# Performance work log

Measured on AMD Instinct MI355X. Metric: run time of the kernel, lower is better.

## Reference

```python
import jax, jax.numpy as jnp
import numpy as np

N = 262144  # points per batch (~4096 rays x 64 samples)
FDIM = 64   # plane feature dim
S = 512     # base plane resolution


def setup_inputs() -> dict:
    key = jax.random.key(0)
    ks = jax.random.split(key, 10)
    x = jax.random.uniform(ks[0], (N, 3), dtype=jnp.float32, minval=-1.0, maxval=1.0)
    rays_o = jnp.array([[0.0, 0.0, 1.5]], dtype=jnp.float32)  # ray origin; distances straddle 1.5/2.0
    scale = jnp.ones((3,), dtype=jnp.float32)
    plane = lambda k, s: jax.random.normal(k, (FDIM, s, s), dtype=jnp.float32)
    return {
        'x': x, 'rays_o': rays_o, 'scale': scale,
        'xy_plane': plane(ks[1], S), 'yz_plane': plane(ks[2], S), 'xz_plane': plane(ks[3], S),
        'xy_plane1': plane(ks[4], S // 2), 'yz_plane1': plane(ks[5], S // 2), 'xz_plane1': plane(ks[6], S // 2),
        'xy_plane2': plane(ks[7], S // 4), 'yz_plane2': plane(ks[8], S // 4), 'xz_plane2': plane(ks[9], S // 4),
    }


def bilinear_sample(plane, coords):
    """F.grid_sample(mode='bilinear', align_corners=True, padding_mode='zeros').
    plane: [C, H, W]; coords: [N, 2] with (x, y) in [-1, 1] (x indexes W).
    Returns [N, C]."""
    C, H, W = plane.shape
    fx = (coords[:, 0] + 1.0) * 0.5 * (W - 1)
    fy = (coords[:, 1] + 1.0) * 0.5 * (H - 1)
    x0 = jnp.floor(fx)
    y0 = jnp.floor(fy)
    wx = fx - x0
    wy = fy - y0
    x0i = x0.astype(jnp.int32)
    y0i = y0.astype(jnp.int32)

    def gather(xi, yi):
        valid = (xi >= 0) & (xi < W) & (yi >= 0) & (yi < H)
        xc = jnp.clip(xi, 0, W - 1)
        yc = jnp.clip(yi, 0, H - 1)
        v = plane[:, yc, xc]  # [C, N]
        return jnp.where(valid[None, :], v, 0.0)

    v00 = gather(x0i, y0i)
    v01 = gather(x0i + 1, y0i)
    v10 = gather(x0i, y0i + 1)
    v11 = gather(x0i + 1, y0i + 1)
    out = (v00 * (1 - wx) * (1 - wy) + v01 * wx * (1 - wy)
           + v10 * (1 - wx) * wy + v11 * wx * wy)  # [C, N]
    return out.T


def forward(x, rays_o, scale, xy0, yz0, xz0, xy1, yz1, xz1, xy2, yz2, xz2):
    xs = x * scale[None, :]
    xy_c = xs[:, :2]                                   # (x, y)
    xz_c = jnp.stack([xs[:, 0], xs[:, 2]], axis=-1)    # (x, z)
    yz_c = xs[:, 1:]                                   # (y, z)

    # laplace breakpoints: first index with distance > 1.5 / > 2.0 from rays_o[0]
    d = jnp.linalg.norm(rays_o[0][None, :] - xs, axis=-1)
    c1 = d > 1.5
    c2 = d > 2.0
    break1 = jnp.where(c1.any(), jnp.argmax(c1), 0)
    break2 = jnp.where(c2.any(), jnp.argmax(c2), 0)
    idx = jnp.arange(x.shape[0])
    # level 0: [0, break1), level 1: [break1, break2), level 2: [break2, N)
    level = jnp.where(idx < break1, 0, jnp.where(idx < break2, 1, 2))[:, None]

    def tri(p0, p1, p2, c):
        s0 = bilinear_sample(p0, c)
        s1 = bilinear_sample(p1, c)
        s2 = bilinear_sample(p2, c)
        # laplace: level1 = fine + half, level2 = fine + half + quarter
        return jnp.where(level == 0, s0, jnp.where(level == 1, s0 + s1, s0 + s1 + s2))

    return (tri(xy0, xy1, xy2, xy_c)
            + tri(xz0, xz1, xz2, xz_c)
            + tri(yz0, yz1, yz2, yz_c))


def reference(x, rays_o, scale, xy_plane, yz_plane, xz_plane, xy_plane1, yz_plane1, xz_plane1, xy_plane2, yz_plane2, xz_plane2):
    return forward(x, rays_o, scale, xy_plane, yz_plane, xz_plane,
                   xy_plane1, yz_plane1, xz_plane1,
                   xy_plane2, yz_plane2, xz_plane2)
```

## Files before the change

### kernel.cpp

```cpp
#include <hip/hip_runtime.h>
#include <hip/hip_fp16.h>

#define NPTS 262144
#define FDIM 64
#define NCELL 32768

typedef float vfloat4 __attribute__((ext_vector_type(4)));

__global__ __launch_bounds__(256) void break_kernel(const float* __restrict__ x,
                                                    const float* __restrict__ rays_o,
                                                    const float* __restrict__ scale,
                                                    unsigned* __restrict__ breaks) {
  const unsigned t = blockIdx.x * 256u + threadIdx.x;
  const float r0 = rays_o[0], r1 = rays_o[1], r2 = rays_o[2];
  const float s0 = scale[0], s1 = scale[1], s2 = scale[2];
  unsigned b1 = 0xFFFFFFFFu, b2 = 0xFFFFFFFFu;
  for (unsigned p = t; p < NPTS; p += 65536u) {
    const float dx = r0 - x[p * 3 + 0] * s0;
    const float dy = r1 - x[p * 3 + 1] * s1;
    const float dz = r2 - x[p * 3 + 2] * s2;
    const float d = sqrtf(__fadd_rn(__fadd_rn(__fmul_rn(dx, dx), __fmul_rn(dy, dy)),
                                    __fmul_rn(dz, dz)));
    if (d > 1.5f) b1 = min(b1, p);
    if (d > 2.0f) b2 = min(b2, p);
  }
  __shared__ unsigned sb1[256];
  __shared__ unsigned sb2[256];
  sb1[threadIdx.x] = b1;
  sb2[threadIdx.x] = b2;
  __syncthreads();
  for (int s = 128; s > 0; s >>= 1) {
    if ((int)threadIdx.x < s) {
      sb1[threadIdx.x] = min(sb1[threadIdx.x], sb1[threadIdx.x + s]);
      sb2[threadIdx.x] = min(sb2[threadIdx.x], sb2[threadIdx.x + s]);
    }
    __syncthreads();
  }
  if (threadIdx.x == 0) {
    atomicMin(&breaks[0], sb1[0]);
    atomicMin(&breaks[1], sb2[0]);
  }
}

__device__ __forceinline__ unsigned part5(unsigned v) {
  v &= 31u;
  v = (v | (v << 8)) & 0x100Fu;
  v = (v | (v << 4)) & 0x10C3u;
  v = (v | (v << 2)) & 0x1249u;
  return v;
}

__device__ __forceinline__ unsigned cell_key(float x0, float x1, float x2) {
  const int cx = min(max((int)((x0 + 1.0f) * 16.0f), 0), 31);
  const int cy = min(max((int)((x1 + 1.0f) * 16.0f), 0), 31);
  const int cz = min(max((int)((x2 + 1.0f) * 16.0f), 0), 31);
  return part5((unsigned)cx) | (part5((unsigned)cy) << 1) | (part5((unsigned)cz) << 2);
}

__global__ __launch_bounds__(256) void hist_kernel(const float* __restrict__ x,
                                                   const float* __restrict__ scale,
                                                   unsigned* __restrict__ hist) {
  const unsigned t = blockIdx.x * 256u + threadIdx.x;
  const float s0 = scale[0], s1 = scale[1], s2 = scale[2];
  const unsigned key = cell_key(x[t * 3 + 0] * s0, x[t * 3 + 1] * s1, x[t * 3 + 2] * s2);
  atomicAdd(&hist[key], 1u);
}

__global__ __launch_bounds__(256) void scan1_kernel(unsigned* __restrict__ hist,
                                                    unsigned* __restrict__ partials) {
  const int cell = blockIdx.x * 256 + threadIdx.x;
  const int tid = threadIdx.x;
  const unsigned h = hist[cell];
  __shared__ unsigned ls[256];
  ls[tid] = h;
  __syncthreads();
  for (int d = 1; d < 256; d <<= 1) {
    const unsigned add = (tid >= d) ? ls[tid - d] : 0u;
    __syncthreads();
    ls[tid] += add;
    __syncthreads();
  }
  hist[cell] = ls[tid] - h;
  if (tid == 255) partials[blockIdx.x] = ls[255];
}

__global__ __launch_bounds__(128) void scan2_kernel(unsigned* __restrict__ partials) {
  const int tid = threadIdx.x;
  const unsigned h = partials[tid];
  __shared__ unsigned ls[128];
  ls[tid] = h;
  __syncthreads();
  for (int d = 1; d < 128; d <<= 1) {
    const unsigned add = (tid >= d) ? ls[tid - d] : 0u;
    __syncthreads();
    ls[tid] += add;
    __syncthreads();
  }
  partials[tid] = ls[tid] - h;
}

__global__ __launch_bounds__(256) void scan3_kernel(unsigned* __restrict__ hist,
                                                    const unsigned* __restrict__ partials) {
  const int cell = blockIdx.x * 256 + threadIdx.x;
  hist[cell] += partials[blockIdx.x];
}

__global__ __launch_bounds__(256) void scatter_kernel(const float* __restrict__ x,
                                                      const float* __restrict__ scale,
                                                      unsigned* __restrict__ offs,
                                                      unsigned* __restrict__ order) {
  const unsigned t = blockIdx.x * 256u + threadIdx.x;
  const float s0 = scale[0], s1 = scale[1], s2 = scale[2];
  const unsigned key = cell_key(x[t * 3 + 0] * s0, x[t * 3 + 1] * s1, x[t * 3 + 2] * s2);
  const unsigned pos = atomicAdd(&offs[key], 1u);
  order[pos] = t;
}

struct TransposeArgs {
  const float* src[9];
  __half* dst[9];
  int tile_hi[9];
  int SS[9];
};

__global__ __launch_bounds__(256) void transpose_all(TransposeArgs a) {
  __shared__ __half lds[256 * 66];
  const int tile = blockIdx.x;
  int pi = 0;
#pragma unroll
  for (int i = 0; i < 9; ++i) {
    if (tile >= a.tile_hi[i]) pi = i + 1;
  }
  const int lo = (pi == 0) ? 0 : a.tile_hi[pi - 1];
  const float* __restrict__ src = a.src[pi];
  __half* __restrict__ dst = a.dst[pi];
  const size_t SS = (size_t)a.SS[pi];
  const size_t p0 = (size_t)(tile - lo) * 256;

  const int t = threadIdx.x;
  const int px4 = t & 63;
  const int cg = t >> 6;
#pragma unroll
  for (int it = 0; it < 16; ++it) {
    const int c = it * 4 + cg;
    const float4 v = *(const float4*)(src + (size_t)c * SS + p0 + (size_t)px4 * 4);
    lds[(px4 * 4 + 0) * 66 + c] = __float2half(v.x);
    lds[(px4 * 4 + 1) * 66 + c] = __float2half(v.y);
    lds[(px4 * 4 + 2) * 66 + c] = __float2half(v.z);
    lds[(px4 * 4 + 3) * 66 + c] = __float2half(v.w);
  }
  __syncthreads();
  const int c8 = t & 7;
  const int pxo = t >> 3;
#pragma unroll
  for (int it = 0; it < 8; ++it) {
    const int px = it * 32 + pxo;
    const unsigned* w = (const unsigned*)(lds + px * 66 + c8 * 8);
    uint4 v;
    v.x = w[0]; v.y = w[1]; v.z = w[2]; v.w = w[3];
    *(uint4*)(dst + (p0 + (size_t)px) * FDIM + c8 * 8) = v;
  }
}

union H8 { uint4 u; __half h[8]; };

__device__ __forceinline__ void bilinear_weights(int W, float cx, float cy,
                                                 float& w00, float& w01, float& w10, float& w11,
                                                 int& xc0, int& xc1, int& yc0, int& yc1) {
  const float Wm1 = (float)(W - 1);
  const float fx = (cx + 1.0f) * 0.5f * Wm1;
  const float fy = (cy + 1.0f) * 0.5f * Wm1;
  const float x0f = floorf(fx), y0f = floorf(fy);
  const float wx = fx - x0f, wy = fy - y0f;
  const int ix = (int)x0f, iy = (int)y0f;
  const int ix1 = ix + 1, iy1 = iy + 1;
  const bool vx0 = (ix >= 0) && (ix < W);
  const bool vx1 = (ix1 >= 0) && (ix1 < W);
  const bool vy0 = (iy >= 0) && (iy < W);
  const bool vy1 = (iy1 >= 0) && (iy1 < W);
  xc0 = min(max(ix, 0), W - 1);
  xc1 = min(max(ix1, 0), W - 1);
  yc0 = min(max(iy, 0), W - 1);
  yc1 = min(max(iy1, 0), W - 1);
  w00 = (1.0f - wx) * (1.0f - wy) * (float)(vx0 && vy0);
  w01 = wx * (1.0f - wy) * (float)(vx1 && vy0);
  w10 = (1.0f - wx) * wy * (float)(vx0 && vy1);
  w11 = wx * wy * (float)(vx1 && vy1);
}

__device__ __forceinline__ void sample8_t(const __half* __restrict__ pl, int W,
                                          float cx, float cy, int j8, float acc[8]) {
  float w00, w01, w10, w11;
  int xc0, xc1, yc0, yc1;
  bilinear_weights(W, cx, cy, w00, w01, w10, w11, xc0, xc1, yc0, yc1);
  const __half* b00 = pl + ((size_t)(yc0 * W + xc0) * FDIM + j8);
  const __half* b01 = pl + ((size_t)(yc0 * W + xc1) * FDIM + j8);
  const __half* b10 = pl + ((size_t)(yc1 * W + xc0) * FDIM + j8);
  const __half* b11 = pl + ((size_t)(yc1 * W + xc1) * FDIM + j8);
  H8 v00, v01, v10, v11;
  v00.u = *(const uint4*)b00;
  v01.u = *(const uint4*)b01;
  v10.u = *(const uint4*)b10;
  v11.u = *(const uint4*)b11;
#pragma unroll
  for (int k = 0; k < 8; ++k) {
    acc[k] += w00 * __half2float(v00.h[k]) + w01 * __half2float(v01.h[k]) +
              w10 * __half2float(v10.h[k]) + w11 * __half2float(v11.h[k]);
  }
}

__device__ __forceinline__ void sample8_d(const float* __restrict__ pl, int W,
                                          float cx, float cy, int j8, float acc[8]) {
  float w00, w01, w10, w11;
  int xc0, xc1, yc0, yc1;
  bilinear_weights(W, cx, cy, w00, w01, w10, w11, xc0, xc1, yc0, yc1);
  const size_t SS = (size_t)W * W;
  const int i00 = yc0 * W + xc0, i01 = yc0 * W + xc1;
  const int i10 = yc1 * W + xc0, i11 = yc1 * W + xc1;
#pragma unroll
  for (int k = 0; k < 8; ++k) {
    const size_t co = (size_t)(j8 + k) * SS;
    acc[k] += w00 * pl[co + i00] + w01 * pl[co + i01] +
              w10 * pl[co + i10] + w11 * pl[co + i11];
  }
}

struct PlanesH { const __half* p[9]; };
struct PlanesF { const float* p[9]; };

__global__ __launch_bounds__(256) void sample_kernel(const float* __restrict__ x,
                                                     const float* __restrict__ scale,
                                                     const unsigned* __restrict__ breaks,
                                                     const unsigned* __restrict__ order,
                                                     PlanesH tp, float* __restrict__ out) {
  const int t = blockIdx.x * 256 + threadIdx.x;
  const int slot = t >> 3;
  const int p = (int)order[slot];
  const int j8 = (t & 7) * 8;
  const float s0 = scale[0], s1 = scale[1], s2 = scale[2];
  const float xs0 = x[p * 3 + 0] * s0;
  const float xs1 = x[p * 3 + 1] * s1;
  const float xs2 = x[p * 3 + 2] * s2;
  unsigned b1 = breaks[0]; if (b1 >= NPTS) b1 = 0;
  unsigned b2 = breaks[1]; if (b2 >= NPTS) b2 = 0;
  const unsigned pu = (unsigned)p;
  const int level = (pu < b1) ? 0 : ((pu < b2) ? 1 : 2);
  float acc[8];
#pragma unroll
  for (int k = 0; k < 8; ++k) acc[k] = 0.0f;
  sample8_t(tp.p[0], 512, xs0, xs1, j8, acc);
  sample8_t(tp.p[1], 512, xs1, xs2, j8, acc);
  sample8_t(tp.p[2], 512, xs0, xs2, j8, acc);
  if (level >= 1) {
    sample8_t(tp.p[3], 256, xs0, xs1, j8, acc);
    sample8_t(tp.p[4], 256, xs1, xs2, j8, acc);
    sample8_t(tp.p[5], 256, xs0, xs2, j8, acc);
  }
  if (level >= 2) {
    sample8_t(tp.p[6], 128, xs0, xs1, j8, acc);
    sample8_t(tp.p[7], 128, xs1, xs2, j8, acc);
    sample8_t(tp.p[8], 128, xs0, xs2, j8, acc);
  }
  float* o = out + (size_t)p * FDIM + j8;
  vfloat4 lo = {acc[0], acc[1], acc[2], acc[3]};
  vfloat4 hi = {acc[4], acc[5], acc[6], acc[7]};
  __builtin_nontemporal_store(lo, (vfloat4*)o);
  __builtin_nontemporal_store(hi, (vfloat4*)(o + 4));
}

__global__ __launch_bounds__(256) void sample_kernel_direct(const float* __restrict__ x,
                                                            const float* __restrict__ scale,
                                                            const unsigned* __restrict__ breaks,
                                                            PlanesF tp, float* __restrict__ out) {
  const int t = blockIdx.x * 256 + threadIdx.x;
  const int p = t >> 3;
  const int j8 = (t & 7) * 8;
  const float s0 = scale[0], s1 = scale[1], s2 = scale[2];
  const float xs0 = x[p * 3 + 0] * s0;
  const float xs1 = x[p * 3 + 1] * s1;
  const float xs2 = x[p * 3 + 2] * s2;
  unsigned b1 = breaks[0]; if (b1 >= NPTS) b1 = 0;
  unsigned b2 = breaks[1]; if (b2 >= NPTS) b2 = 0;
  const unsigned pu = (unsigned)p;
  const int level = (pu < b1) ? 0 : ((pu < b2) ? 1 : 2);
  float acc[8];
#pragma unroll
  for (int k = 0; k < 8; ++k) acc[k] = 0.0f;
  sample8_d(tp.p[0], 512, xs0, xs1, j8, acc);
  sample8_d(tp.p[1], 512, xs1, xs2, j8, acc);
  sample8_d(tp.p[2], 512, xs0, xs2, j8, acc);
  if (level >= 1) {
    sample8_d(tp.p[3], 256, xs0, xs1, j8, acc);
    sample8_d(tp.p[4], 256, xs1, xs2, j8, acc);
    sample8_d(tp.p[5], 256, xs0, xs2, j8, acc);
  }
  if (level >= 2) {
    sample8_d(tp.p[6], 128, xs0, xs1, j8, acc);
    sample8_d(tp.p[7], 128, xs1, xs2, j8, acc);
    sample8_d(tp.p[8], 128, xs0, xs2, j8, acc);
  }
  float4* o4 = (float4*)(out + (size_t)p * FDIM + j8);
  o4[0] = make_float4(acc[0], acc[1], acc[2], acc[3]);
  o4[1] = make_float4(acc[4], acc[5], acc[6], acc[7]);
}

extern "C" void kernel_launch(void* const* d_in, const int* in_sizes, int n_in,
                              void* d_out, int out_size, void* d_ws, size_t ws_size,
                              hipStream_t stream) {
  const float* x = (const float*)d_in[0];
  const float* rays_o = (const float*)d_in[1];
  const float* scale = (const float*)d_in[2];
  const float* pl32[9];
  for (int i = 0; i < 9; ++i) pl32[i] = (const float*)d_in[3 + i];
  float* out = (float*)d_out;

  unsigned char* ws = (unsigned char*)d_ws;
  unsigned* breaks = (unsigned*)ws;
  unsigned* partials = (unsigned*)(ws + 128);
  unsigned* hist = (unsigned*)(ws + 1024);
  unsigned* order = (unsigned*)(ws + 1024 + NCELL * 4);
  const size_t planes_off = 1024 + (size_t)NCELL * 4 + (size_t)NPTS * 4;

  (void)hipMemsetAsync(d_ws, 0xFF, 8, stream);
  break_kernel<<<256, 256, 0, stream>>>(x, rays_o, scale, breaks);

  const int Ss[3] = {512, 256, 128};
  size_t need = planes_off;
  for (int l = 0; l < 3; ++l) need += 3 * (size_t)Ss[l] * Ss[l] * FDIM * sizeof(__half);

  if (ws_size >= need) {
    (void)hipMemsetAsync(hist, 0, NCELL * 4, stream);
    hist_kernel<<<NPTS / 256, 256, 0, stream>>>(x, scale, hist);
    scan1_kernel<<<NCELL / 256, 256, 0, stream>>>(hist, partials);
    scan2_kernel<<<1, 128, 0, stream>>>(partials);
    scan3_kernel<<<NCELL / 256, 256, 0, stream>>>(hist, partials);
    scatter_kernel<<<NPTS / 256, 256, 0, stream>>>(x, scale, hist, order);

    PlanesH tp;
    TransposeArgs ta;
    size_t off = planes_off;
    int tiles_acc = 0;
    for (int l = 0; l < 3; ++l) {
      const int S = Ss[l];
      const int SS = S * S;
      for (int o = 0; o < 3; ++o) {
        const int i = l * 3 + o;
        __half* dst = (__half*)(ws + off);
        tp.p[i] = dst;
        ta.src[i] = pl32[i];
        ta.dst[i] = dst;
        ta.SS[i] = SS;
        tiles_acc += SS / 256;
        ta.tile_hi[i] = tiles_acc;
        off += (size_t)SS * FDIM * sizeof(__half);
      }
    }
    transpose_all<<<tiles_acc, 256, 0, stream>>>(ta);
    sample_kernel<<<(NPTS * 8) / 256, 256, 0, stream>>>(x, scale, breaks, order, tp, out);
  } else {
    PlanesF tf;
    for (int i = 0; i < 9; ++i) tf.p[i] = pl32[i];
    sample_kernel_direct<<<(NPTS * 8) / 256, 256, 0, stream>>>(x, scale, breaks, tf, out);
  }
}
```

Baseline: 429.6 us.

## Fuse break/hist passes, presort scaled coords, LDS-free transpose, XCD block swizzle

Merges the break-distance reduction into the histogram kernel using wavefront shuffles, drops the separate scan-add kernel by adding partials inside scatter, and has scatter write sorted scaled coordinates packed with point index and level into a float4 array. This removes the indirect order lookup and the per-thread level computation in the sampling kernel. The plane transpose now converts directly in registers without shared memory, and sample blocks are remapped so contiguous sorted chunks land on the same XCD for L2 reuse. The coalesced writes in the transpose and the larger sorted buffer trade against fewer launches and passes.

```diff
diff --git a/kernel.cpp b/kernel.cpp
--- a/kernel.cpp
+++ b/kernel.cpp
@@ -24,21 +24,14 @@
     if (d > 1.5f) b1 = min(b1, p);
     if (d > 2.0f) b2 = min(b2, p);
   }
-  __shared__ unsigned sb1[256];
-  __shared__ unsigned sb2[256];
-  sb1[threadIdx.x] = b1;
-  sb2[threadIdx.x] = b2;
-  __syncthreads();
-  for (int s = 128; s > 0; s >>= 1) {
-    if ((int)threadIdx.x < s) {
-      sb1[threadIdx.x] = min(sb1[threadIdx.x], sb1[threadIdx.x + s]);
-      sb2[threadIdx.x] = min(sb2[threadIdx.x], sb2[threadIdx.x + s]);
-    }
-    __syncthreads();
-  }
-  if (threadIdx.x == 0) {
-    atomicMin(&breaks[0], sb1[0]);
-    atomicMin(&breaks[1], sb2[0]);
+#pragma unroll
+  for (int o = 32; o > 0; o >>= 1) {
+    b1 = min(b1, (unsigned)__shfl_down((int)b1, o, 64));
+    b2 = min(b2, (unsigned)__shfl_down((int)b2, o, 64));
+  }
+  if ((threadIdx.x & 63) == 0) {
+    atomicMin(&breaks[0], b1);
+    atomicMin(&breaks[1], b2);
   }
 }
 
@@ -57,12 +50,33 @@
   return part5((unsigned)cx) | (part5((unsigned)cy) << 1) | (part5((unsigned)cz) << 2);
 }
 
-__global__ __launch_bounds__(256) void hist_kernel(const float* __restrict__ x,
-                                                   const float* __restrict__ scale,
-                                                   unsigned* __restrict__ hist) {
+__global__ __launch_bounds__(256) void breakhist_kernel(const float* __restrict__ x,
+                                                        const float* __restrict__ rays_o,
+                                                        const float* __restrict__ scale,
+                                                        unsigned* __restrict__ breaks,
+                                                        unsigned* __restrict__ hist) {
   const unsigned t = blockIdx.x * 256u + threadIdx.x;
   const float s0 = scale[0], s1 = scale[1], s2 = scale[2];
-  const unsigned key = cell_key(x[t * 3 + 0] * s0, x[t * 3 + 1] * s1, x[t * 3 + 2] * s2);
+  const float xs0 = x[t * 3 + 0] * s0;
+  const float xs1 = x[t * 3 + 1] * s1;
+  const float xs2 = x[t * 3 + 2] * s2;
+  const float dx = rays_o[0] - xs0;
+  const float dy = rays_o[1] - xs1;
+  const float dz = rays_o[2] - xs2;
+  const float d = sqrtf(__fadd_rn(__fadd_rn(__fmul_rn(dx, dx), __fmul_rn(dy, dy)),
+                                  __fmul_rn(dz, dz)));
+  unsigned b1 = (d > 1.5f) ? t : 0xFFFFFFFFu;
+  unsigned b2 = (d > 2.0f) ? t : 0xFFFFFFFFu;
+#pragma unroll
+  for (int o = 32; o > 0; o >>= 1) {
+    b1 = min(b1, (unsigned)__shfl_down((int)b1, o, 64));
+    b2 = min(b2, (unsigned)__shfl_down((int)b2, o, 64));
+  }
+  if ((threadIdx.x & 63) == 0) {
+    atomicMin(&breaks[0], b1);
+    atomicMin(&breaks[1], b2);
+  }
+  const unsigned key = cell_key(xs0, xs1, xs2);
   atomicAdd(&hist[key], 1u);
 }
 
@@ -99,22 +113,29 @@
   partials[tid] = ls[tid] - h;
 }
 
-__global__ __launch_bounds__(256) void scan3_kernel(unsigned* __restrict__ hist,
-                                                    const unsigned* __restrict__ partials) {
-  const int cell = blockIdx.x * 256 + threadIdx.x;
-  hist[cell] += partials[blockIdx.x];
-}
-
 __global__ __launch_bounds__(256) void scatter_kernel(const float* __restrict__ x,
                                                       const float* __restrict__ scale,
+                                                      const unsigned* __restrict__ breaks,
                                                       unsigned* __restrict__ offs,
-                                                      unsigned* __restrict__ order) {
+                                                      const unsigned* __restrict__ partials,
+                                                      float4* __restrict__ xs_sorted) {
   const unsigned t = blockIdx.x * 256u + threadIdx.x;
   const float s0 = scale[0], s1 = scale[1], s2 = scale[2];
-  const unsigned key = cell_key(x[t * 3 + 0] * s0, x[t * 3 + 1] * s1, x[t * 3 + 2] * s2);
-  const unsigned pos = atomicAdd(&offs[key], 1u);
-  order[pos] = t;
-}
+  const float xs0 = x[t * 3 + 0] * s0;
+  const float xs1 = x[t * 3 + 1] * s1;
+  const float xs2 = x[t * 3 + 2] * s2;
+  const unsigned key = cell_key(xs0, xs1, xs2);
+  const unsigned pos = atomicAdd(&offs[key], 1u) + partials[key >> 8];
+  unsigned b1 = breaks[0]; if (b1 >= NPTS) b1 = 0;
+  unsigned b2 = breaks[1]; if (b2 >= NPTS) b2 = 0;
+  const unsigned lvl = (t < b1) ? 0u : ((t < b2) ? 1u : 2u);
+  float4 v;
+  v.x = xs0; v.y = xs1; v.z = xs2;
+  v.w = __uint_as_float(t | (lvl << 18));
+  xs_sorted[pos] = v;
+}
+
+#define TPIX 128
 
 struct TransposeArgs {
   const float* src[9];
@@ -123,8 +144,9 @@
   int SS[9];
 };
 
+union H8 { uint4 u; __half h[8]; };
+
 __global__ __launch_bounds__(256) void transpose_all(TransposeArgs a) {
-  __shared__ __half lds[256 * 66];
   const int tile = blockIdx.x;
   int pi = 0;
 #pragma unroll
@@ -135,34 +157,27 @@
   const float* __restrict__ src = a.src[pi];
   __half* __restrict__ dst = a.dst[pi];
   const size_t SS = (size_t)a.SS[pi];
-  const size_t p0 = (size_t)(tile - lo) * 256;
 
   const int t = threadIdx.x;
-  const int px4 = t & 63;
-  const int cg = t >> 6;
-#pragma unroll
-  for (int it = 0; it < 16; ++it) {
-    const int c = it * 4 + cg;
-    const float4 v = *(const float4*)(src + (size_t)c * SS + p0 + (size_t)px4 * 4);
-    lds[(px4 * 4 + 0) * 66 + c] = __float2half(v.x);
-    lds[(px4 * 4 + 1) * 66 + c] = __float2half(v.y);
-    lds[(px4 * 4 + 2) * 66 + c] = __float2half(v.z);
-    lds[(px4 * 4 + 3) * 66 + c] = __float2half(v.w);
-  }
-  __syncthreads();
+  const int slot = t >> 3;
   const int c8 = t & 7;
-  const int pxo = t >> 3;
-#pragma unroll
-  for (int it = 0; it < 8; ++it) {
-    const int px = it * 32 + pxo;
-    const unsigned* w = (const unsigned*)(lds + px * 66 + c8 * 8);
-    uint4 v;
-    v.x = w[0]; v.y = w[1]; v.z = w[2]; v.w = w[3];
-    *(uint4*)(dst + (p0 + (size_t)px) * FDIM + c8 * 8) = v;
-  }
-}
-
-union H8 { uint4 u; __half h[8]; };
+  const size_t p0 = (size_t)(tile - lo) * TPIX + (size_t)slot * 4;
+  const float* __restrict__ srcb = src + (size_t)(c8 * 8) * SS + p0;
+
+  H8 h[4];
+#pragma unroll
+  for (int k = 0; k < 8; ++k) {
+    const float4 v = *(const float4*)(srcb + (size_t)k * SS);
+    h[0].h[k] = __float2half(v.x);
+    h[1].h[k] = __float2half(v.y);
+    h[2].h[k] = __float2half(v.z);
+    h[3].h[k] = __float2half(v.w);
+  }
+#pragma unroll
+  for (int r = 0; r < 4; ++r) {
+    *(uint4*)(dst + (p0 + (size_t)r) * FDIM + c8 * 8) = h[r].u;
+  }
+}
 
 __device__ __forceinline__ void bilinear_weights(int W, float cx, float cy,
                                                  float& w00, float& w01, float& w10, float& w11,
@@ -228,38 +243,35 @@
 struct PlanesH { const __half* p[9]; };
 struct PlanesF { const float* p[9]; };
 
-__global__ __launch_bounds__(256) void sample_kernel(const float* __restrict__ x,
-                                                     const float* __restrict__ scale,
-                                                     const unsigned* __restrict__ breaks,
-                                                     const unsigned* __restrict__ order,
+#define SAMPLE_BLOCKS (NPTS * 8 / 256)
+#define XCD_CHUNK (SAMPLE_BLOCKS / 8)
+
+__global__ __launch_bounds__(256) void sample_kernel(const float4* __restrict__ xs_sorted,
                                                      PlanesH tp, float* __restrict__ out) {
-  const int t = blockIdx.x * 256 + threadIdx.x;
+  const unsigned b = blockIdx.x;
+  const unsigned sb = (b & 7u) * XCD_CHUNK + (b >> 3);
+  const int t = (int)(sb * 256u + threadIdx.x);
   const int slot = t >> 3;
-  const int p = (int)order[slot];
   const int j8 = (t & 7) * 8;
-  const float s0 = scale[0], s1 = scale[1], s2 = scale[2];
-  const float xs0 = x[p * 3 + 0] * s0;
-  const float xs1 = x[p * 3 + 1] * s1;
-  const float xs2 = x[p * 3 + 2] * s2;
-  unsigned b1 = breaks[0]; if (b1 >= NPTS) b1 = 0;
-  unsigned b2 = breaks[1]; if (b2 >= NPTS) b2 = 0;
-  const unsigned pu = (unsigned)p;
-  const int level = (pu < b1) ? 0 : ((pu < b2) ? 1 : 2);
+  const float4 ps = xs_sorted[slot];
+  const unsigned w = __float_as_uint(ps.w);
+  const int p = (int)(w & 0x3FFFFu);
+  const int level = (int)(w >> 18);
   float acc[8];
 #pragma unroll
   for (int k = 0; k < 8; ++k) acc[k] = 0.0f;
-  sample8_t(tp.p[0], 512, xs0, xs1, j8, acc);
-  sample8_t(tp.p[1], 512, xs1, xs2, j8, acc);
-  sample8_t(tp.p[2], 512, xs0, xs2, j8, acc);
+  sample8_t(tp.p[0], 512, ps.x, ps.y, j8, acc);
+  sample8_t(tp.p[1], 512, ps.y, ps.z, j8, acc);
+  sample8_t(tp.p[2], 512, ps.x, ps.z, j8, acc);
   if (level >= 1) {
-    sample8_t(tp.p[3], 256, xs0, xs1, j8, acc);
-    sample8_t(tp.p[4], 256, xs1, xs2, j8, acc);
-    sample8_t(tp.p[5], 256, xs0, xs2, j8, acc);
+    sample8_t(tp.p[3], 256, ps.x, ps.y, j8, acc);
+    sample8_t(tp.p[4], 256, ps.y, ps.z, j8, acc);
+    sample8_t(tp.p[5], 256, ps.x, ps.z, j8, acc);
   }
   if (level >= 2) {
-    sample8_t(tp.p[6], 128, xs0, xs1, j8, acc);
-    sample8_t(tp.p[7], 128, xs1, xs2, j8, acc);
-    sample8_t(tp.p[8], 128, xs0, xs2, j8, acc);
+    sample8_t(tp.p[6], 128, ps.x, ps.y, j8, acc);
+    sample8_t(tp.p[7], 128, ps.y, ps.z, j8, acc);
+    sample8_t(tp.p[8], 128, ps.x, ps.z, j8, acc);
   }
   float* o = out + (size_t)p * FDIM + j8;
   vfloat4 lo = {acc[0], acc[1], acc[2], acc[3]};
@@ -318,11 +330,10 @@
   unsigned* breaks = (unsigned*)ws;
   unsigned* partials = (unsigned*)(ws + 128);
   unsigned* hist = (unsigned*)(ws + 1024);
-  unsigned* order = (unsigned*)(ws + 1024 + NCELL * 4);
-  const size_t planes_off = 1024 + (size_t)NCELL * 4 + (size_t)NPTS * 4;
+  float4* xs_sorted = (float4*)(ws + 1024 + NCELL * 4);
+  const size_t planes_off = 1024 + (size_t)NCELL * 4 + (size_t)NPTS * 16;
 
   (void)hipMemsetAsync(d_ws, 0xFF, 8, stream);
-  break_kernel<<<256, 256, 0, stream>>>(x, rays_o, scale, breaks);
 
   const int Ss[3] = {512, 256, 128};
   size_t need = planes_off;
@@ -330,11 +341,10 @@
 
   if (ws_size >= need) {
     (void)hipMemsetAsync(hist, 0, NCELL * 4, stream);
-    hist_kernel<<<NPTS / 256, 256, 0, stream>>>(x, scale, hist);
+    breakhist_kernel<<<NPTS / 256, 256, 0, stream>>>(x, rays_o, scale, breaks, hist);
     scan1_kernel<<<NCELL / 256, 256, 0, stream>>>(hist, partials);
     scan2_kernel<<<1, 128, 0, stream>>>(partials);
-    scan3_kernel<<<NCELL / 256, 256, 0, stream>>>(hist, partials);
-    scatter_kernel<<<NPTS / 256, 256, 0, stream>>>(x, scale, hist, order);
+    scatter_kernel<<<NPTS / 256, 256, 0, stream>>>(x, scale, breaks, hist, partials, xs_sorted);
 
     PlanesH tp;
     TransposeArgs ta;
@@ -350,14 +360,15 @@
         ta.src[i] = pl32[i];
         ta.dst[i] = dst;
         ta.SS[i] = SS;
-        tiles_acc += SS / 256;
+        tiles_acc += SS / TPIX;
         ta.tile_hi[i] = tiles_acc;
         off += (size_t)SS * FDIM * sizeof(__half);
       }
     }
     transpose_all<<<tiles_acc, 256, 0, stream>>>(ta);
-    sample_kernel<<<(NPTS * 8) / 256, 256, 0, stream>>>(x, scale, breaks, order, tp, out);
+    sample_kernel<<<SAMPLE_BLOCKS, 256, 0, stream>>>(xs_sorted, tp, out);
   } else {
+    break_kernel<<<256, 256, 0, stream>>>(x, rays_o, scale, breaks);
     PlanesF tf;
     for (int i = 0; i < 9; ++i) tf.p[i] = pl32[i];
     sample_kernel_direct<<<(NPTS * 8) / 256, 256, 0, stream>>>(x, scale, breaks, tf, out);
```

Measured after the change: 490.4 us. +14.2%, slower.
